# Performance work log

Measured on AMD Instinct MI355X. Metric: run time of the kernel, lower is better.

Reference implementation:

```python
import jax, jax.numpy as jnp
import numpy as np

NEG_SLOPE = 0.01
EPS = 1e-5


def leaky_relu(x):
    return jnp.where(x >= 0, x, NEG_SLOPE * x)


def graph_conv(x, W, src, dst, edge_weight, num_nodes):
    # DGL GraphConv, norm='both', bias=False: D_out^{-1/2} A_w D_in^{-1/2} X W
    ones = jnp.ones_like(edge_weight)
    deg_out = jnp.maximum(jax.ops.segment_sum(ones, src, num_segments=num_nodes), 1.0)
    deg_in = jnp.maximum(jax.ops.segment_sum(ones, dst, num_segments=num_nodes), 1.0)
    h = x @ W
    h = h * jax.lax.rsqrt(deg_out)[:, None]
    agg = jax.ops.segment_sum(h[src] * edge_weight[:, None], dst, num_segments=num_nodes)
    return agg * jax.lax.rsqrt(deg_in)[:, None]


def graph_norm(x, alpha, gamma, beta, batch_size):
    # GraphNorm: per-graph, per-channel mean/var; graphs are equal-sized -> reshape
    n = x.shape[0] // batch_size
    xg = x.reshape(batch_size, n, x.shape[1])
    mean = xg.mean(axis=1, keepdims=True)
    sub = xg - alpha * mean
    var = (sub * sub).mean(axis=1, keepdims=True)
    out = gamma * sub * jax.lax.rsqrt(var + EPS) + beta
    return out.reshape(x.shape)


def instance_norm(x):
    # InstanceNorm1d (affine=False) on 2D input: per-row normalization over features
    mean = x.mean(axis=-1, keepdims=True)
    var = ((x - mean) ** 2).mean(axis=-1, keepdims=True)
    return (x - mean) * jax.lax.rsqrt(var + EPS)


def setup_inputs() -> dict:
    key = jax.random.key(0)
    ks = jax.random.split(key, 9)
    B, n = 4096, 64                      # graphs, nodes per graph (equal-sized)
    N = B * n                            # 262144 nodes
    E = 8 * N                            # avg degree 8
    in_feats, conv_dim, out_conv = 64, 128, 96
    in_mlp = out_conv * n                # 6144 = in_feats_mlp
    hid = 2048
    out_feats = 256

    def kaiming(k, fin, fout):
        bound = float(np.sqrt(6.0 / ((1 + NEG_SLOPE ** 2) * fin)))
        return jax.random.uniform(k, (fin, fout), jnp.float32, -bound, bound)

    def xavier(k, fin, fout):
        bound = float(np.sqrt(6.0 / (fin + fout)))
        return jax.random.uniform(k, (fin, fout), jnp.float32, -bound, bound)

    return {
        "x": jax.random.normal(ks[0], (N, in_feats), jnp.float32),
        "edge_weight": jax.random.uniform(ks[1], (E,), jnp.float32),
        "src": jax.random.randint(ks[2], (E,), 0, N, jnp.int32),
        "dst": jax.random.randint(ks[3], (E,), 0, N, jnp.int32),
        "W1": kaiming(ks[4], in_feats, conv_dim),
        "W2": kaiming(ks[5], conv_dim, out_conv),
        "gn1_alpha": jnp.ones((conv_dim,), jnp.float32),
        "gn1_gamma": jnp.ones((conv_dim,), jnp.float32),
        "gn1_beta": jnp.zeros((conv_dim,), jnp.float32),
        "gn2_alpha": jnp.ones((out_conv,), jnp.float32),
        "gn2_gamma": jnp.ones((out_conv,), jnp.float32),
        "gn2_beta": jnp.zeros((out_conv,), jnp.float32),
        "Win": xavier(ks[6], in_mlp, hid),
        "Whid": xavier(ks[7], hid, hid // 4),
        "Wcls": xavier(ks[8], hid // 4, out_feats),
        "batch_size": B,
    }


def reference(x, edge_weight, src, dst, W1, W2, gn1_alpha, gn1_gamma, gn1_beta,
              gn2_alpha, gn2_gamma, gn2_beta, Win, Whid, Wcls, batch_size):
    N = x.shape[0]
    h = graph_conv(x, W1, src, dst, edge_weight, N)
    h = leaky_relu(h)
    h = graph_norm(h, gn1_alpha, gn1_gamma, gn1_beta, batch_size)
    h = graph_conv(h, W2, src, dst, edge_weight, N)
    h = leaky_relu(h)
    h = graph_norm(h, gn2_alpha, gn2_gamma, gn2_beta, batch_size)
    # unbatch: each equal-size graph flattened to one row [B, n*out_conv]
    h = h.reshape(batch_size, -1)
    h = instance_norm(leaky_relu(h @ Win))   # dropout is identity (p=0 / eval)
    h = instance_norm(leaky_relu(h @ Whid))
    return h @ Wcls
```

## Files before the change

kernel.cpp:

```cpp
#include <hip/hip_runtime.h>
#include <hip/hip_bf16.h>

#define NN 262144
#define EE 2097152
#define BB 4096
constexpr int INMLP = 6144;
constexpr int HID = 2048;
constexpr int HID4 = 512;
constexpr int OUTF = 256;
constexpr int NSL = 64;
constexpr int ESL = EE / NSL;
constexpr int RNODES = 32768;

typedef short s16x8 __attribute__((ext_vector_type(8)));
typedef short s16x4 __attribute__((ext_vector_type(4)));
typedef float f32x4 __attribute__((ext_vector_type(4)));

__device__ __forceinline__ float lrelu(float v) { return v >= 0.f ? v : 0.01f * v; }
__device__ __forceinline__ float bf2f(short s) {
    unsigned int u = ((unsigned int)(unsigned short)s) << 16;
    return __builtin_bit_cast(float, u);
}
__device__ __forceinline__ short f2bf(float f) {
    unsigned int u = __builtin_bit_cast(unsigned int, f);
    u = (u + 0x7fff + ((u >> 16) & 1)) >> 16;
    return (short)u;
}
__device__ __forceinline__ void async16(const void* g, void* l) {
    __builtin_amdgcn_global_load_lds((__attribute__((address_space(1))) void*)g,
                                     (__attribute__((address_space(3))) void*)l, 16, 0, 0);
}

__global__ __launch_bounds__(256) void hist_count(const int* __restrict__ dst, const int* __restrict__ src,
                                                  unsigned* __restrict__ part_din, unsigned* __restrict__ part_dout,
                                                  unsigned short* __restrict__ rankpack16) {
    __shared__ unsigned hist[RNODES / 2];
    const int S = blockIdx.x & 63;
    const int R = (blockIdx.x >> 6) & 7;
    const int T = blockIdx.x >> 9;
    for (int i = threadIdx.x; i < RNODES / 2; i += 256) hist[i] = 0;
    __syncthreads();
    const int* idxarr = T ? src : dst;
    const int4* v4 = (const int4*)(idxarr + S * ESL);
#pragma unroll 4
    for (int i = 0; i < ESL / 4 / 256; i++) {
        const int q0 = i * 256 + threadIdx.x;
        int4 q = v4[q0];
        const int ebase = S * ESL + q0 * 4;
#pragma unroll
        for (int k = 0; k < 4; k++) {
            int idx = k == 0 ? q.x : k == 1 ? q.y : k == 2 ? q.z : q.w;
            if ((idx >> 15) == R) {
                int local = idx & (RNODES - 1);
                unsigned old = atomicAdd(&hist[local >> 1], 1u << ((local & 1) * 16));
                if (T == 0) {
                    unsigned rank = (old >> ((local & 1) * 16)) & 0xffffu;
                    rankpack16[ebase + k] = (unsigned short)((S << 10) | rank);
                }
            }
        }
    }
    __syncthreads();
    unsigned* dp = (T ? part_dout : part_din) + (size_t)S * (NN / 2) + R * (RNODES / 2);
    for (int i = threadIdx.x; i < RNODES / 2; i += 256) dp[i] = hist[i];
}

__global__ __launch_bounds__(256) void deg_reduce(const unsigned* __restrict__ part_din,
                                                  const unsigned* __restrict__ part_dout,
                                                  unsigned* __restrict__ repbase_w,
                                                  float* __restrict__ ro, float* __restrict__ ri,
                                                  int* __restrict__ din) {
    int i = blockIdx.x * 256 + threadIdx.x;
    unsigned runl = 0, runh = 0, dl = 0, dh = 0;
#pragma unroll 8
    for (int S = 0; S < NSL; S++) {
        repbase_w[(size_t)S * (NN / 2) + i] = (runl & 0xffffu) | (runh << 16);
        unsigned w = part_din[(size_t)S * (NN / 2) + i];
        runl += w & 0xffffu; runh += w >> 16;
        unsigned w2 = part_dout[(size_t)S * (NN / 2) + i];
        dl += w2 & 0xffffu; dh += w2 >> 16;
    }
    int n0 = 2 * i, n1 = 2 * i + 1;
    din[n0] = (int)runl; din[n1] = (int)runh;
    ro[n0] = rsqrtf((float)(dl < 1u ? 1u : dl));
    ro[n1] = rsqrtf((float)(dh < 1u ? 1u : dh));
    ri[n0] = rsqrtf((float)(runl < 1u ? 1u : runl));
    ri[n1] = rsqrtf((float)(runh < 1u ? 1u : runh));
}

__global__ __launch_bounds__(256) void scanA(const int* __restrict__ cnt, int* __restrict__ blks) {
    __shared__ int s[256];
    int t = threadIdx.x;
    int i0 = blockIdx.x * 1024 + t * 4;
    int ts = cnt[i0] + cnt[i0 + 1] + cnt[i0 + 2] + cnt[i0 + 3];
    s[t] = ts; __syncthreads();
    for (int d = 128; d > 0; d >>= 1) { if (t < d) s[t] += s[t + d]; __syncthreads(); }
    if (t == 0) blks[blockIdx.x] = s[0];
}

__global__ __launch_bounds__(256) void scanB(int* __restrict__ blks, int* __restrict__ offN) {
    __shared__ int s[256];
    int t = threadIdx.x;
    int v = blks[t]; s[t] = v; __syncthreads();
    for (int d = 1; d < 256; d <<= 1) {
        int x = (t >= d) ? s[t - d] : 0; __syncthreads();
        s[t] += x; __syncthreads();
    }
    blks[t] = s[t] - v;
    if (t == 255) *offN = s[255];
}

__global__ __launch_bounds__(256) void scanC(const int* __restrict__ cnt, const int* __restrict__ blkoff,
                                             int* __restrict__ off) {
    __shared__ int s[256];
    int t = threadIdx.x;
    int i0 = blockIdx.x * 1024 + t * 4;
    int v0 = cnt[i0], v1 = cnt[i0 + 1], v2 = cnt[i0 + 2], v3 = cnt[i0 + 3];
    int ts = v0 + v1 + v2 + v3;
    s[t] = ts; __syncthreads();
    for (int d = 1; d < 256; d <<= 1) {
        int x = (t >= d) ? s[t - d] : 0; __syncthreads();
        s[t] += x; __syncthreads();
    }
    int base = blkoff[blockIdx.x] + (s[t] - ts);
    off[i0] = base; off[i0 + 1] = base + v0; off[i0 + 2] = base + v0 + v1; off[i0 + 3] = base + v0 + v1 + v2;
}

__global__ __launch_bounds__(256) void fill_csr(const int* __restrict__ src, const int* __restrict__ dst,
                                                const float* __restrict__ ew, const float* __restrict__ ro,
                                                const int* __restrict__ off,
                                                const unsigned short* __restrict__ repbase16,
                                                const unsigned short* __restrict__ rankpack16,
                                                int2* __restrict__ edg) {
    int e = blockIdx.x * 256 + threadIdx.x;
    int d = dst[e];
    int s = src[e];
    unsigned pk = rankpack16[e];
    int S = pk >> 10, rank = pk & 1023;
    int p = off[d] + (int)repbase16[(size_t)S * NN + d] + rank;
    edg[p] = make_int2(s, __builtin_bit_cast(int, ew[e] * ro[s]));
}

__global__ __launch_bounds__(256) void cvt_x(const float* __restrict__ X, short* __restrict__ Xb) {
    int i = (blockIdx.x * 256 + threadIdx.x) * 4;
    float4 v = *(const float4*)(X + i);
    s16x4 o = { f2bf(v.x), f2bf(v.y), f2bf(v.z), f2bf(v.w) };
    *(s16x4*)(Xb + i) = o;
}

__global__ __launch_bounds__(256) void gather64(const short* __restrict__ Xb, const int* __restrict__ offs,
                                                const int2* __restrict__ edg, short* __restrict__ Out) {
    const int lane = threadIdx.x & 63;
    const int e = lane >> 3, c = lane & 7;
    int node = blockIdx.x * 4 + (threadIdx.x >> 6);
    node = __builtin_amdgcn_readfirstlane(node);
    const int s0 = offs[node], s1 = offs[node + 1];
    float acc[8] = {};
    for (int j0 = s0; j0 < s1; j0 += 8) {
        int j = j0 + e;
        bool ok = j < s1;
        int2 pe = edg[ok ? j : s0];
        int s = pe.x;
        float w = ok ? __builtin_bit_cast(float, pe.y) : 0.f;
        s16x8 v = *(const s16x8*)&Xb[(size_t)s * 64 + c * 8];
#pragma unroll
        for (int k = 0; k < 8; k++) acc[k] = fmaf(w, bf2f(v[k]), acc[k]);
    }
#pragma unroll
    for (int off = 8; off <= 32; off <<= 1)
#pragma unroll
        for (int k = 0; k < 8; k++) acc[k] += __shfl_xor(acc[k], off);
    if (e == 0) {
        s16x8 o;
#pragma unroll
        for (int k = 0; k < 8; k++) o[k] = f2bf(acc[k]);
        *(s16x8*)&Out[(size_t)node * 64 + c * 8] = o;
    }
}

__global__ __launch_bounds__(256) void conv1_gn(const short* __restrict__ A, const short* __restrict__ BT,
                                                const float* __restrict__ ri,
                                                const float* __restrict__ alpha, const float* __restrict__ gamma,
                                                const float* __restrict__ beta, short* __restrict__ Outp) {
    __shared__ short As[128][72];
    __shared__ short Bs[128][72];
    __shared__ float sscale[2][128], sshift[2][128];
    const int t = threadIdx.x;
    const int bm = blockIdx.x * 128;
    const int wave = t >> 6, lane = t & 63;
    const int wm = (wave & 1) * 64, wn = (wave >> 1) * 64;
    const int g = wave & 1;
    const int m16 = lane & 15, quad = lane >> 4;
#pragma unroll
    for (int i = 0; i < 4; i++) {
        int idx = t + 256 * i;
        int rr = idx >> 3, kk = (idx & 7) * 8;
        *(s16x8*)&As[rr][kk] = *(const s16x8*)&A[(size_t)(bm + rr) * 64 + kk];
        *(s16x8*)&Bs[rr][kk] = *(const s16x8*)&BT[(size_t)rr * 64 + kk];
    }
    __syncthreads();
    f32x4 acc[4][4] = {};
#pragma unroll
    for (int kc = 0; kc < 2; kc++) {
        s16x8 af[4], bfr[4];
#pragma unroll
        for (int mt = 0; mt < 4; mt++) af[mt] = *(const s16x8*)&As[wm + mt * 16 + m16][kc * 32 + quad * 8];
#pragma unroll
        for (int nt = 0; nt < 4; nt++) bfr[nt] = *(const s16x8*)&Bs[wn + nt * 16 + m16][kc * 32 + quad * 8];
#pragma unroll
        for (int mt = 0; mt < 4; mt++)
#pragma unroll
            for (int nt = 0; nt < 4; nt++)
                acc[mt][nt] = __builtin_amdgcn_mfma_f32_16x16x32_bf16(af[mt], bfr[nt], acc[mt][nt], 0, 0, 0);
    }
#pragma unroll
    for (int mt = 0; mt < 4; mt++)
#pragma unroll
        for (int r4 = 0; r4 < 4; r4++) {
            float rv = ri[bm + wm + mt * 16 + quad * 4 + r4];
#pragma unroll
            for (int nt = 0; nt < 4; nt++)
                acc[mt][nt][r4] = lrelu(acc[mt][nt][r4] * rv);
        }
#pragma unroll
    for (int nt = 0; nt < 4; nt++) {
        float s1 = 0.f, s2 = 0.f;
#pragma unroll
        for (int mt = 0; mt < 4; mt++)
#pragma unroll
            for (int r4 = 0; r4 < 4; r4++) { float v = acc[mt][nt][r4]; s1 += v; s2 += v * v; }
        s1 += __shfl_xor(s1, 16); s1 += __shfl_xor(s1, 32);
        s2 += __shfl_xor(s2, 16); s2 += __shfl_xor(s2, 32);
        if (quad == 0) {
            int ch = wn + nt * 16 + m16;
            float m = s1 * (1.f / 64.f);
            float a = alpha[ch];
            float var = s2 * (1.f / 64.f) - m * m * a * (2.f - a);
            float sc = gamma[ch] * rsqrtf(var + 1e-5f);
            sscale[g][ch] = sc;
            sshift[g][ch] = beta[ch] - sc * a * m;
        }
    }
    __syncthreads();
#pragma unroll
    for (int nt = 0; nt < 4; nt++) {
        int ch = wn + nt * 16 + m16;
        float sc = sscale[g][ch], sh = sshift[g][ch];
#pragma unroll
        for (int mt = 0; mt < 4; mt++)
#pragma unroll
            for (int r4 = 0; r4 < 4; r4++) {
                int row = bm + wm + mt * 16 + quad * 4 + r4;
                Outp[(size_t)row * 128 + ch] = f2bf(sc * acc[mt][nt][r4] + sh);
            }
    }
}

__global__ __launch_bounds__(256) void conv2_mfma(const short* __restrict__ A, const short* __restrict__ BT,
                                                  short* __restrict__ H) {
    __shared__ short As[128][136];
    __shared__ short Bs[96][136];
    const int t = threadIdx.x;
    const int bm = blockIdx.x * 128;
    const int wave = t >> 6, lane = t & 63;
    const int wm = (wave & 1) * 64, wn = (wave >> 1) * 48;
    const int m16 = lane & 15, quad = lane >> 4;
#pragma unroll
    for (int i = 0; i < 8; i++) {
        int idx = t + 256 * i;
        int rr = idx >> 4, kk = (idx & 15) * 8;
        *(s16x8*)&As[rr][kk] = *(const s16x8*)&A[(size_t)(bm + rr) * 128 + kk];
    }
#pragma unroll
    for (int i = 0; i < 6; i++) {
        int idx = t + 256 * i;
        int nr = idx >> 4, kk = (idx & 15) * 8;
        *(s16x8*)&Bs[nr][kk] = *(const s16x8*)&BT[(size_t)nr * 128 + kk];
    }
    __syncthreads();
    f32x4 acc[4][3] = {};
#pragma unroll
    for (int kc = 0; kc < 4; kc++) {
        s16x8 af[4], bfr[3];
#pragma unroll
        for (int mt = 0; mt < 4; mt++) af[mt] = *(const s16x8*)&As[wm + mt * 16 + m16][kc * 32 + quad * 8];
#pragma unroll
        for (int nt = 0; nt < 3; nt++) bfr[nt] = *(const s16x8*)&Bs[wn + nt * 16 + m16][kc * 32 + quad * 8];
#pragma unroll
        for (int mt = 0; mt < 4; mt++)
#pragma unroll
            for (int nt = 0; nt < 3; nt++)
                acc[mt][nt] = __builtin_amdgcn_mfma_f32_16x16x32_bf16(af[mt], bfr[nt], acc[mt][nt], 0, 0, 0);
    }
#pragma unroll
    for (int mt = 0; mt < 4; mt++)
#pragma unroll
        for (int r4 = 0; r4 < 4; r4++) {
            int row = bm + wm + mt * 16 + quad * 4 + r4;
#pragma unroll
            for (int nt = 0; nt < 3; nt++)
                H[(size_t)row * 96 + wn + nt * 16 + m16] = f2bf(acc[mt][nt][r4]);
        }
}

__global__ __launch_bounds__(256) void gather_gn2(const short* __restrict__ H, const int* __restrict__ offs,
                                                  const int2* __restrict__ edg,
                                                  const float* __restrict__ ri,
                                                  const float* __restrict__ alpha, const float* __restrict__ gamma,
                                                  const float* __restrict__ beta, short* __restrict__ Outp) {
    __shared__ float sm[64 * 96];
    __shared__ float sscale[96], sshift[96];
    const int g = blockIdx.x;
    const int wave = threadIdx.x >> 6, lane = threadIdx.x & 63;
    const int e = lane >> 4, c = lane & 15;
    for (int nl = wave * 16; nl < wave * 16 + 16; nl++) {
        const int node = g * 64 + nl;
        const int s0 = offs[node], s1 = offs[node + 1];
        float acc[6] = {};
        for (int j0 = s0; j0 < s1; j0 += 4) {
            int j = j0 + e;
            bool ok = j < s1;
            int2 pe = edg[ok ? j : s0];
            int s = pe.x;
            float w = ok ? __builtin_bit_cast(float, pe.y) : 0.f;
            const unsigned int* hp = (const unsigned int*)(H + (size_t)s * 96 + c * 6);
            unsigned int u0 = hp[0], u1 = hp[1], u2 = hp[2];
            acc[0] = fmaf(w, bf2f((short)(u0 & 0xffff)), acc[0]);
            acc[1] = fmaf(w, bf2f((short)(u0 >> 16)), acc[1]);
            acc[2] = fmaf(w, bf2f((short)(u1 & 0xffff)), acc[2]);
            acc[3] = fmaf(w, bf2f((short)(u1 >> 16)), acc[3]);
            acc[4] = fmaf(w, bf2f((short)(u2 & 0xffff)), acc[4]);
            acc[5] = fmaf(w, bf2f((short)(u2 >> 16)), acc[5]);
        }
#pragma unroll
        for (int off = 16; off <= 32; off <<= 1)
#pragma unroll
            for (int k = 0; k < 6; k++) acc[k] += __shfl_xor(acc[k], off);
        if (e == 0) {
            float rv = ri[node];
#pragma unroll
            for (int k = 0; k < 6; k++) sm[nl * 96 + c * 6 + k] = lrelu(acc[k] * rv);
        }
    }
    __syncthreads();
    if (threadIdx.x < 96) {
        int cch = threadIdx.x;
        float s1v = 0.f, s2v = 0.f;
#pragma unroll 4
        for (int i = 0; i < 64; i++) { float v = sm[i * 96 + cch]; s1v += v; s2v += v * v; }
        float m = s1v * (1.f / 64.f);
        float a = alpha[cch];
        float var = s2v * (1.f / 64.f) - m * m * a * (2.f - a);
        float sc = gamma[cch] * rsqrtf(var + 1e-5f);
        sscale[cch] = sc;
        sshift[cch] = beta[cch] - sc * a * m;
    }
    __syncthreads();
#pragma unroll
    for (int i = 0; i < 6; i++) {
        int q = threadIdx.x + 256 * i;
        int nl = q / 24, cq = (q % 24) * 4;
        s16x4 o;
#pragma unroll
        for (int k = 0; k < 4; k++) o[k] = f2bf(sscale[cq + k] * sm[nl * 96 + cq + k] + sshift[cq + k]);
        *(s16x4*)&Outp[(size_t)(g * 64 + nl) * 96 + cq] = o;
    }
}

__global__ __launch_bounds__(256) void transp_cvt(const float* __restrict__ W, short* __restrict__ WT,
                                                  int R, int Cc) {
    __shared__ short tile[32][33];
    const int bc = blockIdx.x * 32;
    const int br = blockIdx.y * 32;
    const int tx = threadIdx.x & 31, ty = threadIdx.x >> 5;
#pragma unroll
    for (int i = 0; i < 32; i += 8)
        tile[ty + i][tx] = f2bf(W[(size_t)(br + ty + i) * Cc + bc + tx]);
    __syncthreads();
#pragma unroll
    for (int i = 0; i < 32; i += 8)
        WT[(size_t)(bc + ty + i) * R + br + tx] = tile[tx][ty + i];
}

__global__ __launch_bounds__(256) void mlp1_mfma(const short* __restrict__ A, const short* __restrict__ BT,
                                                 float* __restrict__ C) {
    constexpr int K = INMLP, Nn = HID;
    __shared__ short As[128 * 64];
    __shared__ short Bs[128 * 64];
    const int t = threadIdx.x;
    const int bm = blockIdx.x * 128, bn = blockIdx.y * 128;
    const int wave = t >> 6, lane = t & 63;
    const int wm = (wave & 1) * 64, wn = (wave >> 1) * 64;
    const int m16 = lane & 15, quad = lane >> 4;
    const int lrow = lane >> 3, lcol = lane & 7;
    const int scol = lcol ^ (lrow & 7);
    const int xkey = m16 & 7;
    f32x4 acc[4][4] = {};
    for (int k0 = 0; k0 < K; k0 += 64) {
#pragma unroll
        for (int j = 0; j < 4; j++) {
            const int rbase = 32 * wave + 8 * j;
            async16(&A[(size_t)(bm + rbase + lrow) * K + k0 + scol * 8], &As[rbase * 64]);
            async16(&BT[(size_t)(bn + rbase + lrow) * K + k0 + scol * 8], &Bs[rbase * 64]);
        }
        __syncthreads();
#pragma unroll
        for (int kc = 0; kc < 2; kc++) {
            s16x8 af[4], bfr[4];
#pragma unroll
            for (int mt = 0; mt < 4; mt++)
                af[mt] = *(const s16x8*)&As[(wm + mt * 16 + m16) * 64 + (((kc * 4 + quad) ^ xkey)) * 8];
#pragma unroll
            for (int nt = 0; nt < 4; nt++)
                bfr[nt] = *(const s16x8*)&Bs[(wn + nt * 16 + m16) * 64 + (((kc * 4 + quad) ^ xkey)) * 8];
#pragma unroll
            for (int mt = 0; mt < 4; mt++)
#pragma unroll
                for (int nt = 0; nt < 4; nt++)
                    acc[mt][nt] = __builtin_amdgcn_mfma_f32_16x16x32_bf16(af[mt], bfr[nt], acc[mt][nt], 0, 0, 0);
        }
        __syncthreads();
    }
#pragma unroll
    for (int mt = 0; mt < 4; mt++)
#pragma unroll
        for (int nt = 0; nt < 4; nt++)
#pragma unroll
            for (int r4 = 0; r4 < 4; r4++) {
                int row = bm + wm + mt * 16 + quad * 4 + r4;
                int col = bn + wn + nt * 16 + m16;
                C[(size_t)row * Nn + col] = lrelu(acc[mt][nt][r4]);
            }
}

template <bool LEAKY>
__global__ __launch_bounds__(256) void mfma_gemm_af32(const float* __restrict__ A, const short* __restrict__ BT,
                                                      float* __restrict__ C, int M, int Nn, int K) {
    __shared__ short As[64][40];
    __shared__ short Bs[64][40];
    const int t = threadIdx.x;
    const int bm = blockIdx.x * 64, bn = blockIdx.y * 64;
    const int wave = t >> 6, lane = t & 63;
    const int wm = (wave & 1) * 32, wn = (wave >> 1) * 32;
    const int m16 = lane & 15, quad = lane >> 4;
    const int rr = t >> 2, kk = (t & 3) * 8;
    f32x4 acc[2][2] = {};
    for (int k0 = 0; k0 < K; k0 += 32) {
        const float* ap = &A[(size_t)(bm + rr) * K + k0 + kk];
        float4 v0 = *(const float4*)ap;
        float4 v1 = *(const float4*)(ap + 4);
        s16x8 a8;
        a8[0] = f2bf(v0.x); a8[1] = f2bf(v0.y); a8[2] = f2bf(v0.z); a8[3] = f2bf(v0.w);
        a8[4] = f2bf(v1.x); a8[5] = f2bf(v1.y); a8[6] = f2bf(v1.z); a8[7] = f2bf(v1.w);
        *(s16x8*)&As[rr][kk] = a8;
        *(s16x8*)&Bs[rr][kk] = *(const s16x8*)&BT[(size_t)(bn + rr) * K + k0 + kk];
        __syncthreads();
        s16x8 af[2], bfr[2];
#pragma unroll
        for (int mt = 0; mt < 2; mt++) af[mt] = *(const s16x8*)&As[wm + mt * 16 + m16][quad * 8];
#pragma unroll
        for (int nt = 0; nt < 2; nt++) bfr[nt] = *(const s16x8*)&Bs[wn + nt * 16 + m16][quad * 8];
#pragma unroll
        for (int mt = 0; mt < 2; mt++)
#pragma unroll
            for (int nt = 0; nt < 2; nt++)
                acc[mt][nt] = __builtin_amdgcn_mfma_f32_16x16x32_bf16(af[mt], bfr[nt], acc[mt][nt], 0, 0, 0);
        __syncthreads();
    }
#pragma unroll
    for (int mt = 0; mt < 2; mt++)
#pragma unroll
        for (int nt = 0; nt < 2; nt++)
#pragma unroll
            for (int r4 = 0; r4 < 4; r4++) {
                int row = bm + wm + mt * 16 + quad * 4 + r4;
                int col = bn + wn + nt * 16 + m16;
                float v = acc[mt][nt][r4];
                if (LEAKY) v = lrelu(v);
                C[(size_t)row * Nn + col] = v;
            }
}

template <int NC>
__global__ __launch_bounds__(256) void rownorm(float* __restrict__ Y) {
    float* p = Y + (size_t)blockIdx.x * NC;
    float s1 = 0.f, s2 = 0.f;
    for (int c = threadIdx.x; c < NC; c += 256) { float v = p[c]; s1 += v; s2 += v * v; }
#pragma unroll
    for (int o = 32; o > 0; o >>= 1) { s1 += __shfl_down(s1, o); s2 += __shfl_down(s2, o); }
    __shared__ float w1[4], w2[4];
    if ((threadIdx.x & 63) == 0) { w1[threadIdx.x >> 6] = s1; w2[threadIdx.x >> 6] = s2; }
    __syncthreads();
    s1 = w1[0] + w1[1] + w1[2] + w1[3];
    s2 = w2[0] + w2[1] + w2[2] + w2[3];
    float m = s1 * (1.f / NC);
    float inv = rsqrtf(s2 * (1.f / NC) - m * m + 1e-5f);
    for (int c = threadIdx.x; c < NC; c += 256) p[c] = (p[c] - m) * inv;
}

extern "C" void kernel_launch(void* const* d_in, const int* in_sizes, int n_in,
                              void* d_out, int out_size, void* d_ws, size_t ws_size,
                              hipStream_t stream) {
    const float* x    = (const float*)d_in[0];
    const float* ew   = (const float*)d_in[1];
    const int*   src  = (const int*)d_in[2];
    const int*   dst  = (const int*)d_in[3];
    const float* W1   = (const float*)d_in[4];
    const float* W2   = (const float*)d_in[5];
    const float* a1   = (const float*)d_in[6];
    const float* g1   = (const float*)d_in[7];
    const float* b1   = (const float*)d_in[8];
    const float* a2   = (const float*)d_in[9];
    const float* g2   = (const float*)d_in[10];
    const float* b2   = (const float*)d_in[11];
    const float* Win  = (const float*)d_in[12];
    const float* Whid = (const float*)d_in[13];
    const float* Wcls = (const float*)d_in[14];
    float* out = (float*)d_out;

    float* ro   = (float*)d_ws;
    float* ri   = ro + NN;
    int*   din  = (int*)(ri + NN);
    int*   offs = din + NN;
    int*   blks = offs + NN + 4;
    short* w1t  = (short*)(blks + 256);
    short* w2t  = w1t + 128 * 64;
    int2*  edg  = (int2*)(((size_t)(w2t + 96 * 128) + 15) & ~(size_t)15);
    short* Abf  = (short*)(edg + EE);
    short* Bbf  = Abf + (size_t)NN * 128;
    short* xbf  = Abf;
    short* aggx = Abf + (size_t)NN * 64;
    unsigned*       part_din   = (unsigned*)Abf;
    unsigned*       part_dout  = part_din + (size_t)NSL * (NN / 2);
    unsigned*       repbase_w  = (unsigned*)Bbf;
    unsigned short* rankpack16 = (unsigned short*)(repbase_w + (size_t)NSL * (NN / 2));
    short* WinT = Abf;
    float* D    = (float*)((char*)Abf + 25165824);
    float* Y2   = (float*)((char*)Abf + 25165824 + 33554432);
    short* WhidT = Bbf;
    short* WclsT = WhidT + (size_t)HID4 * HID;

    hist_count<<<2 * 8 * NSL, 256, 0, stream>>>(dst, src, part_din, part_dout, rankpack16);
    deg_reduce<<<NN / 512, 256, 0, stream>>>(part_din, part_dout, repbase_w, ro, ri, din);

    scanA<<<NN / 1024, 256, 0, stream>>>(din, blks);
    scanB<<<1, 256, 0, stream>>>(blks, offs + NN);
    scanC<<<NN / 1024, 256, 0, stream>>>(din, blks, offs);
    fill_csr<<<EE / 256, 256, 0, stream>>>(src, dst, ew, ro, offs,
                                           (const unsigned short*)repbase_w, rankpack16, edg);

    cvt_x<<<NN * 64 / 1024, 256, 0, stream>>>(x, xbf);
    transp_cvt<<<dim3(128 / 32, 64 / 32), 256, 0, stream>>>(W1, w1t, 64, 128);
    gather64<<<NN / 4, 256, 0, stream>>>(xbf, offs, edg, aggx);
    conv1_gn<<<NN / 128, 256, 0, stream>>>(aggx, w1t, ri, a1, g1, b1, Bbf);

    transp_cvt<<<dim3(96 / 32, 128 / 32), 256, 0, stream>>>(W2, w2t, 128, 96);
    conv2_mfma<<<NN / 128, 256, 0, stream>>>(Bbf, w2t, Abf);
    gather_gn2<<<BB, 256, 0, stream>>>(Abf, offs, edg, ri, a2, g2, b2, Bbf);

    transp_cvt<<<dim3(HID / 32, INMLP / 32), 256, 0, stream>>>(Win, WinT, INMLP, HID);
    mlp1_mfma<<<dim3(BB / 128, HID / 128), 256, 0, stream>>>(Bbf, WinT, D);
    transp_cvt<<<dim3(HID4 / 32, HID / 32), 256, 0, stream>>>(Whid, WhidT, HID, HID4);
    transp_cvt<<<dim3(OUTF / 32, HID4 / 32), 256, 0, stream>>>(Wcls, WclsT, HID4, OUTF);
    rownorm<HID><<<BB, 256, 0, stream>>>(D);
    mfma_gemm_af32<true><<<dim3(BB / 64, HID4 / 64), 256, 0, stream>>>(D, WhidT, Y2, BB, HID4, HID);
    rownorm<HID4><<<BB, 256, 0, stream>>>(Y2);
    mfma_gemm_af32<false><<<dim3(BB / 64, OUTF / 64), 256, 0, stream>>>(Y2, WclsT, out, BB, OUTF, HID4);
}
```

Before: 843.0 us.

## Split-K the big MLP GEMM and decouple the second gather from GraphNorm

The large MLP1 GEMM is split along K into two halves (grid z=2) that write bf16 partial results, and a new row-norm kernel sums the halves, applies leaky ReLU and instance norm, then writes bf16 for the next GEMM, which now reads bf16 directly. The fused gather+GraphNorm2 kernel, which used one block per graph, is split into a per-node gather kernel with four nodes per block and a separate GraphNorm kernel. The aim is more parallelism for the 32x16-block GEMM and for the gather, plus less fp32 traffic, at the cost of extra launches, an extra pass over the gathered features, and bf16 rounding of the partial sums.

Result: no change. 833.1 us (-1.2%).

```diff
diff --git a/kernel.cpp b/kernel.cpp
--- a/kernel.cpp
+++ b/kernel.cpp
@@ -178,6 +178,74 @@
     }
 }
 
+__global__ __launch_bounds__(256) void gather96(const short* __restrict__ H, const int* __restrict__ offs,
+                                                const int2* __restrict__ edg, short* __restrict__ Out) {
+    const int lane = threadIdx.x & 63;
+    const int e = lane >> 4, c = lane & 15;
+    int node = blockIdx.x * 4 + (threadIdx.x >> 6);
+    node = __builtin_amdgcn_readfirstlane(node);
+    const int s0 = offs[node], s1 = offs[node + 1];
+    float acc[6] = {};
+    for (int j0 = s0; j0 < s1; j0 += 4) {
+        int j = j0 + e;
+        bool ok = j < s1;
+        int2 pe = edg[ok ? j : s0];
+        int s = pe.x;
+        float w = ok ? __builtin_bit_cast(float, pe.y) : 0.f;
+        const unsigned int* hp = (const unsigned int*)(H + (size_t)s * 96 + c * 6);
+        unsigned int u0 = hp[0], u1 = hp[1], u2 = hp[2];
+        acc[0] = fmaf(w, bf2f((short)(u0 & 0xffff)), acc[0]);
+        acc[1] = fmaf(w, bf2f((short)(u0 >> 16)), acc[1]);
+        acc[2] = fmaf(w, bf2f((short)(u1 & 0xffff)), acc[2]);
+        acc[3] = fmaf(w, bf2f((short)(u1 >> 16)), acc[3]);
+        acc[4] = fmaf(w, bf2f((short)(u2 & 0xffff)), acc[4]);
+        acc[5] = fmaf(w, bf2f((short)(u2 >> 16)), acc[5]);
+    }
+#pragma unroll
+    for (int off = 16; off <= 32; off <<= 1)
+#pragma unroll
+        for (int k = 0; k < 6; k++) acc[k] += __shfl_xor(acc[k], off);
+    if (e == 0) {
+        unsigned int* op = (unsigned int*)(Out + (size_t)node * 96 + c * 6);
+        op[0] = (unsigned short)f2bf(acc[0]) | ((unsigned)(unsigned short)f2bf(acc[1]) << 16);
+        op[1] = (unsigned short)f2bf(acc[2]) | ((unsigned)(unsigned short)f2bf(acc[3]) << 16);
+        op[2] = (unsigned short)f2bf(acc[4]) | ((unsigned)(unsigned short)f2bf(acc[5]) << 16);
+    }
+}
+
+template <int C>
+__global__ __launch_bounds__(256) void graphnorm_k(short* __restrict__ Ag, const float* __restrict__ ri,
+                                                   const float* __restrict__ alpha, const float* __restrict__ gamma,
+                                                   const float* __restrict__ beta) {
+    __shared__ float sm[64 * C];
+    __shared__ float sscale[C], sshift[C];
+    const int g = blockIdx.x;
+    const size_t base = (size_t)g * 64 * C;
+    for (int idx = threadIdx.x; idx < 64 * C; idx += 256) {
+        int i = idx / C;
+        float v = bf2f(Ag[base + idx]) * ri[g * 64 + i];
+        sm[idx] = lrelu(v);
+    }
+    __syncthreads();
+    if (threadIdx.x < C) {
+        int c = threadIdx.x;
+        float s1 = 0.f, s2 = 0.f;
+#pragma unroll 4
+        for (int i = 0; i < 64; i++) { float v = sm[i * C + c]; s1 += v; s2 += v * v; }
+        float m = s1 * (1.f / 64.f);
+        float a = alpha[c];
+        float var = s2 * (1.f / 64.f) - m * m * a * (2.f - a);
+        float sc = gamma[c] * rsqrtf(var + 1e-5f);
+        sscale[c] = sc;
+        sshift[c] = beta[c] - sc * a * m;
+    }
+    __syncthreads();
+    for (int idx = threadIdx.x; idx < 64 * C; idx += 256) {
+        int c = idx % C;
+        Ag[base + idx] = f2bf(sscale[c] * sm[idx] + sshift[c]);
+    }
+}
+
 __global__ __launch_bounds__(256) void conv1_gn(const short* __restrict__ A, const short* __restrict__ BT,
                                                 const float* __restrict__ ri,
                                                 const float* __restrict__ alpha, const float* __restrict__ gamma,
@@ -303,70 +371,6 @@
         }
 }
 
-__global__ __launch_bounds__(256) void gather_gn2(const short* __restrict__ H, const int* __restrict__ offs,
-                                                  const int2* __restrict__ edg,
-                                                  const float* __restrict__ ri,
-                                                  const float* __restrict__ alpha, const float* __restrict__ gamma,
-                                                  const float* __restrict__ beta, short* __restrict__ Outp) {
-    __shared__ float sm[64 * 96];
-    __shared__ float sscale[96], sshift[96];
-    const int g = blockIdx.x;
-    const int wave = threadIdx.x >> 6, lane = threadIdx.x & 63;
-    const int e = lane >> 4, c = lane & 15;
-    for (int nl = wave * 16; nl < wave * 16 + 16; nl++) {
-        const int node = g * 64 + nl;
-        const int s0 = offs[node], s1 = offs[node + 1];
-        float acc[6] = {};
-        for (int j0 = s0; j0 < s1; j0 += 4) {
-            int j = j0 + e;
-            bool ok = j < s1;
-            int2 pe = edg[ok ? j : s0];
-            int s = pe.x;
-            float w = ok ? __builtin_bit_cast(float, pe.y) : 0.f;
-            const unsigned int* hp = (const unsigned int*)(H + (size_t)s * 96 + c * 6);
-            unsigned int u0 = hp[0], u1 = hp[1], u2 = hp[2];
-            acc[0] = fmaf(w, bf2f((short)(u0 & 0xffff)), acc[0]);
-            acc[1] = fmaf(w, bf2f((short)(u0 >> 16)), acc[1]);
-            acc[2] = fmaf(w, bf2f((short)(u1 & 0xffff)), acc[2]);
-            acc[3] = fmaf(w, bf2f((short)(u1 >> 16)), acc[3]);
-            acc[4] = fmaf(w, bf2f((short)(u2 & 0xffff)), acc[4]);
-            acc[5] = fmaf(w, bf2f((short)(u2 >> 16)), acc[5]);
-        }
-#pragma unroll
-        for (int off = 16; off <= 32; off <<= 1)
-#pragma unroll
-            for (int k = 0; k < 6; k++) acc[k] += __shfl_xor(acc[k], off);
-        if (e == 0) {
-            float rv = ri[node];
-#pragma unroll
-            for (int k = 0; k < 6; k++) sm[nl * 96 + c * 6 + k] = lrelu(acc[k] * rv);
-        }
-    }
-    __syncthreads();
-    if (threadIdx.x < 96) {
-        int cch = threadIdx.x;
-        float s1v = 0.f, s2v = 0.f;
-#pragma unroll 4
-        for (int i = 0; i < 64; i++) { float v = sm[i * 96 + cch]; s1v += v; s2v += v * v; }
-        float m = s1v * (1.f / 64.f);
-        float a = alpha[cch];
-        float var = s2v * (1.f / 64.f) - m * m * a * (2.f - a);
-        float sc = gamma[cch] * rsqrtf(var + 1e-5f);
-        sscale[cch] = sc;
-        sshift[cch] = beta[cch] - sc * a * m;
-    }
-    __syncthreads();
-#pragma unroll
-    for (int i = 0; i < 6; i++) {
-        int q = threadIdx.x + 256 * i;
-        int nl = q / 24, cq = (q % 24) * 4;
-        s16x4 o;
-#pragma unroll
-        for (int k = 0; k < 4; k++) o[k] = f2bf(sscale[cq + k] * sm[nl * 96 + cq + k] + sshift[cq + k]);
-        *(s16x4*)&Outp[(size_t)(g * 64 + nl) * 96 + cq] = o;
-    }
-}
-
 __global__ __launch_bounds__(256) void transp_cvt(const float* __restrict__ W, short* __restrict__ WT,
                                                   int R, int Cc) {
     __shared__ short tile[32][33];
@@ -383,12 +387,13 @@
 }
 
 __global__ __launch_bounds__(256) void mlp1_mfma(const short* __restrict__ A, const short* __restrict__ BT,
-                                                 float* __restrict__ C) {
+                                                 short* __restrict__ Cp) {
     constexpr int K = INMLP, Nn = HID;
     __shared__ short As[128 * 64];
     __shared__ short Bs[128 * 64];
     const int t = threadIdx.x;
     const int bm = blockIdx.x * 128, bn = blockIdx.y * 128;
+    const int kbase = blockIdx.z * (K / 2);
     const int wave = t >> 6, lane = t & 63;
     const int wm = (wave & 1) * 64, wn = (wave >> 1) * 64;
     const int m16 = lane & 15, quad = lane >> 4;
@@ -396,7 +401,7 @@
     const int scol = lcol ^ (lrow & 7);
     const int xkey = m16 & 7;
     f32x4 acc[4][4] = {};
-    for (int k0 = 0; k0 < K; k0 += 64) {
+    for (int k0 = kbase; k0 < kbase + K / 2; k0 += 64) {
 #pragma unroll
         for (int j = 0; j < 4; j++) {
             const int rbase = 32 * wave + 8 * j;
@@ -421,6 +426,7 @@
         }
         __syncthreads();
     }
+    short* C = Cp + (size_t)blockIdx.z * BB * HID;
 #pragma unroll
     for (int mt = 0; mt < 4; mt++)
 #pragma unroll
@@ -429,13 +435,43 @@
             for (int r4 = 0; r4 < 4; r4++) {
                 int row = bm + wm + mt * 16 + quad * 4 + r4;
                 int col = bn + wn + nt * 16 + m16;
-                C[(size_t)row * Nn + col] = lrelu(acc[mt][nt][r4]);
+                C[(size_t)row * Nn + col] = f2bf(acc[mt][nt][r4]);
             }
 }
 
-template <bool LEAKY>
-__global__ __launch_bounds__(256) void mfma_gemm_af32(const float* __restrict__ A, const short* __restrict__ BT,
-                                                      float* __restrict__ C, int M, int Nn, int K) {
+__global__ __launch_bounds__(256) void rownorm_hid(short* __restrict__ D0, const short* __restrict__ D1) {
+    const size_t base = (size_t)blockIdx.x * HID;
+    float v[8];
+    float s1 = 0.f, s2 = 0.f;
+    const int c0 = threadIdx.x * 8;
+    {
+        s16x8 a = *(const s16x8*)&D0[base + c0];
+        s16x8 b = *(const s16x8*)&D1[base + c0];
+#pragma unroll
+        for (int k = 0; k < 8; k++) {
+            float x = lrelu(bf2f(a[k]) + bf2f(b[k]));
+            v[k] = x; s1 += x; s2 += x * x;
+        }
+    }
+#pragma unroll
+    for (int o = 32; o > 0; o >>= 1) { s1 += __shfl_down(s1, o); s2 += __shfl_down(s2, o); }
+    __shared__ float w1[4], w2[4];
+    if ((threadIdx.x & 63) == 0) { w1[threadIdx.x >> 6] = s1; w2[threadIdx.x >> 6] = s2; }
+    __syncthreads();
+    s1 = w1[0] + w1[1] + w1[2] + w1[3];
+    s2 = w2[0] + w2[1] + w2[2] + w2[3];
+    float m = s1 * (1.f / HID);
+    float inv = rsqrtf(s2 * (1.f / HID) - m * m + 1e-5f);
+    s16x8 o;
+#pragma unroll
+    for (int k = 0; k < 8; k++) o[k] = f2bf((v[k] - m) * inv);
+    *(s16x8*)&D0[base + c0] = o;
+}
+
+template <bool ABF16, bool LEAKY>
+__global__ __launch_bounds__(256) void mfma_gemm(const float* __restrict__ Af, const short* __restrict__ Ab,
+                                                 const short* __restrict__ BT,
+                                                 float* __restrict__ C, int M, int Nn, int K) {
     __shared__ short As[64][40];
     __shared__ short Bs[64][40];
     const int t = threadIdx.x;
@@ -446,13 +482,17 @@
     const int rr = t >> 2, kk = (t & 3) * 8;
     f32x4 acc[2][2] = {};
     for (int k0 = 0; k0 < K; k0 += 32) {
-        const float* ap = &A[(size_t)(bm + rr) * K + k0 + kk];
-        float4 v0 = *(const float4*)ap;
-        float4 v1 = *(const float4*)(ap + 4);
-        s16x8 a8;
-        a8[0] = f2bf(v0.x); a8[1] = f2bf(v0.y); a8[2] = f2bf(v0.z); a8[3] = f2bf(v0.w);
-        a8[4] = f2bf(v1.x); a8[5] = f2bf(v1.y); a8[6] = f2bf(v1.z); a8[7] = f2bf(v1.w);
-        *(s16x8*)&As[rr][kk] = a8;
+        if (ABF16) {
+            *(s16x8*)&As[rr][kk] = *(const s16x8*)&Ab[(size_t)(bm + rr) * K + k0 + kk];
+        } else {
+            const float* ap = &Af[(size_t)(bm + rr) * K + k0 + kk];
+            float4 v0 = *(const float4*)ap;
+            float4 v1 = *(const float4*)(ap + 4);
+            s16x8 a8;
+            a8[0] = f2bf(v0.x); a8[1] = f2bf(v0.y); a8[2] = f2bf(v0.z); a8[3] = f2bf(v0.w);
+            a8[4] = f2bf(v1.x); a8[5] = f2bf(v1.y); a8[6] = f2bf(v1.z); a8[7] = f2bf(v1.w);
+            *(s16x8*)&As[rr][kk] = a8;
+        }
         *(s16x8*)&Bs[rr][kk] = *(const s16x8*)&BT[(size_t)(bn + rr) * K + k0 + kk];
         __syncthreads();
         s16x8 af[2], bfr[2];
@@ -535,8 +575,9 @@
     unsigned*       repbase_w  = (unsigned*)Bbf;
     unsigned short* rankpack16 = (unsigned short*)(repbase_w + (size_t)NSL * (NN / 2));
     short* WinT = Abf;
-    float* D    = (float*)((char*)Abf + 25165824);
-    float* Y2   = (float*)((char*)Abf + 25165824 + 33554432);
+    short* D0   = (short*)((char*)Abf + 25165824);
+    short* D1   = D0 + (size_t)BB * HID;
+    float* Y2   = (float*)edg;
     short* WhidT = Bbf;
     short* WclsT = WhidT + (size_t)HID4 * HID;
 
@@ -556,14 +597,15 @@
 
     transp_cvt<<<dim3(96 / 32, 128 / 32), 256, 0, stream>>>(W2, w2t, 128, 96);
     conv2_mfma<<<NN / 128, 256, 0, stream>>>(Bbf, w2t, Abf);
-    gather_gn2<<<BB, 256, 0, stream>>>(Abf, offs, edg, ri, a2, g2, b2, Bbf);
+    gather96<<<NN / 4, 256, 0, stream>>>(Abf, offs, edg, Bbf);
+    graphnorm_k<96><<<BB, 256, 0, stream>>>(Bbf, ri, a2, g2, b2);
 
     transp_cvt<<<dim3(HID / 32, INMLP / 32), 256, 0, stream>>>(Win, WinT, INMLP, HID);
-    mlp1_mfma<<<dim3(BB / 128, HID / 128), 256, 0, stream>>>(Bbf, WinT, D);
+    mlp1_mfma<<<dim3(BB / 128, HID / 128, 2), 256, 0, stream>>>(Bbf, WinT, D0);
     transp_cvt<<<dim3(HID4 / 32, HID / 32), 256, 0, stream>>>(Whid, WhidT, HID, HID4);
     transp_cvt<<<dim3(OUTF / 32, HID4 / 32), 256, 0, stream>>>(Wcls, WclsT, HID4, OUTF);
-    rownorm<HID><<<BB, 256, 0, stream>>>(D);
-    mfma_gemm_af32<true><<<dim3(BB / 64, HID4 / 64), 256, 0, stream>>>(D, WhidT, Y2, BB, HID4, HID);
+    rownorm_hid<<<BB, 256, 0, stream>>>(D0, D1);
+    mfma_gemm<true, true><<<dim3(BB / 64, HID4 / 64), 256, 0, stream>>>(nullptr, D0, WhidT, Y2, BB, HID4, HID);
     rownorm<HID4><<<BB, 256, 0, stream>>>(Y2);
-    mfma_gemm_af32<false><<<dim3(BB / 64, OUTF / 64), 256, 0, stream>>>(Y2, WclsT, out, BB, OUTF, HID4);
-}
+    mfma_gemm<false, false><<<dim3(BB / 64, OUTF / 64), 256, 0, stream>>>(Y2, nullptr, WclsT, out, BB, OUTF, HID4);
+}
```
